# Optimization experiments

Hardware: AMD Instinct MI355X
Metric: run time of the kernel (lower is better)

The kernel has to match this reference:

```python
import jax, jax.numpy as jnp
import numpy as np
from jax import lax

C = 128
HEADS = 8
HID = 256  # int(C * 2.0)
B, H, W = 8, 128, 128
EPS_LN = 1e-5
EPS_NORM = 1e-12


def _dwconv(x, w, pad):
    # x: [B,C,H,W], w: [C,1,kh,kw] depthwise
    return lax.conv_general_dilated(
        x, w, window_strides=(1, 1), padding=[(pad, pad), (pad, pad)],
        dimension_numbers=("NCHW", "OIHW", "NCHW"), feature_group_count=x.shape[1])


def _conv1x1(x, w):
    # w: [O, I] pointwise conv
    return jnp.einsum("oi,bihw->bohw", w, x)


def _layernorm_c(x, gamma, beta):
    # torch: reshape to [B, HW, C], LayerNorm over C, reshape back == LN over channel axis
    mu = jnp.mean(x, axis=1, keepdims=True)
    var = jnp.mean(jnp.square(x - mu), axis=1, keepdims=True)
    xn = (x - mu) * lax.rsqrt(var + EPS_LN)
    return xn * gamma[None, :, None, None] + beta[None, :, None, None]


def _l2norm(x):
    n = jnp.sqrt(jnp.sum(jnp.square(x), axis=-1, keepdims=True))
    return x / jnp.maximum(n, EPS_NORM)


def _mdta(x, qkv_w, qkv_dw, temperature, attn_proj):
    b, c, h, w = x.shape
    qkv = _dwconv(_conv1x1(x, qkv_w), qkv_dw, pad=1)  # [B,3C,H,W]
    q, k, v = jnp.split(qkv, 3, axis=1)
    hd = c // HEADS
    q = q.reshape(b, HEADS, hd, h * w)
    k = k.reshape(b, HEADS, hd, h * w)
    v = v.reshape(b, HEADS, hd, h * w)
    q, k = _l2norm(q), _l2norm(k)
    attn = jax.nn.softmax(jnp.einsum("bhdn,bhen->bhde", q, k) * temperature, axis=-1)
    out = jnp.einsum("bhde,bhen->bhdn", attn, v).reshape(b, c, h, w)
    return _conv1x1(out, attn_proj)


def _gdfn2(x, pin_w, c1_w, c3_w, c5_w, pout_w):
    x = _conv1x1(x, pin_w)  # [B,HID,H,W]
    x1 = x * c1_w[None, :, 0, 0, 0, None, None]  # depthwise 1x1 == per-channel scale
    x3 = _dwconv(x, c3_w, pad=1)
    x5 = _dwconv(x, c5_w, pad=2)
    g = jax.nn.gelu(x1, approximate=False)
    gated = jnp.concatenate([g * x3, g * x5], axis=1)  # [B,2*HID,H,W]
    return _conv1x1(gated, pout_w)


def setup_inputs() -> dict:
    key = jax.random.key(0)
    ks = jax.random.split(key, 12)
    s = 0.05
    return {
        "x": jax.random.normal(ks[0], (B, C, H, W), jnp.float32),
        "ln1_w": jnp.ones((C,), jnp.float32),
        "ln1_b": jnp.zeros((C,), jnp.float32),
        "qkv_w": jax.random.normal(ks[1], (3 * C, C), jnp.float32) * s,
        "qkv_dw": jax.random.normal(ks[2], (3 * C, 1, 3, 3), jnp.float32) * s,
        "temperature": jnp.ones((1, HEADS, 1, 1), jnp.float32),
        "attn_proj": jax.random.normal(ks[3], (C, C), jnp.float32) * s,
        "ln2_w": jnp.ones((C,), jnp.float32),
        "ln2_b": jnp.zeros((C,), jnp.float32),
        "pin_w": jax.random.normal(ks[4], (HID, C), jnp.float32) * s,
        "c1_w": jax.random.normal(ks[5], (HID, 1, 1, 1), jnp.float32) * s,
        "c3_w": jax.random.normal(ks[6], (HID, 1, 3, 3), jnp.float32) * s,
        "c5_w": jax.random.normal(ks[7], (HID, 1, 5, 5), jnp.float32) * s,
        "pout_w": jax.random.normal(ks[8], (C, 2 * HID), jnp.float32) * s,
    }


def reference(x, ln1_w, ln1_b, qkv_w, qkv_dw, temperature, attn_proj,
              ln2_w, ln2_b, pin_w, c1_w, c3_w, c5_w, pout_w):
    x = x + _mdta(_layernorm_c(x, ln1_w, ln1_b), qkv_w, qkv_dw, temperature, attn_proj)
    x = x + _gdfn2(_layernorm_c(x, ln2_w, ln2_b), pin_w, c1_w, c3_w, c5_w, pout_w)
    return x
```

## Files before the change

kernel.cpp:

```cpp
#include <hip/hip_runtime.h>
#include <type_traits>

typedef unsigned short ushort;
typedef unsigned int uint;
typedef __bf16 bf16x8 __attribute__((ext_vector_type(8)));
typedef unsigned short ushort8v __attribute__((ext_vector_type(8)));
typedef float f32x4 __attribute__((ext_vector_type(4)));

__device__ __forceinline__ float b2f(ushort u) {
    unsigned int x = ((unsigned int)u) << 16;
    float f;
    __builtin_memcpy(&f, &x, 4);
    return f;
}
__device__ __forceinline__ ushort f2bf(float f) {
    unsigned int x;
    __builtin_memcpy(&x, &f, 4);
    unsigned int r = x + 0x7fffu + ((x >> 16) & 1u);
    return (ushort)(r >> 16);
}
__device__ __forceinline__ float u2f_lo(uint u) {
    uint x = u << 16;
    float f;
    __builtin_memcpy(&f, &x, 4);
    return f;
}
__device__ __forceinline__ float u2f_hi(uint u) {
    uint x = u & 0xffff0000u;
    float f;
    __builtin_memcpy(&f, &x, 4);
    return f;
}
__device__ __forceinline__ uint packbf(float a, float b) {
    return (uint)f2bf(a) | ((uint)f2bf(b) << 16);
}

#define NPIX 16384
#define PSTRIDE 136

__device__ __forceinline__ size_t tadr(int b, int CH, int tile, int ch, int off) {
    return (((size_t)b * 256 + tile) * CH + ch) * 64 + off;
}
__device__ __forceinline__ size_t padr(int b, int tile, int p, int c) {
    return (((size_t)b * 256 + tile) * 64 + p) * 128 + c;
}

__device__ __forceinline__ void stage_plane(ushort* pl, const ushort* __restrict__ src,
                                            int b, int c, int CH, int tid) {
    uint* plu = (uint*)pl;
    for (int i = tid; i < 784; i += 256) {
        int idx;
        if (i < 136) idx = i;
        else if (i < 272) idx = 8840 + (i - 136);
        else {
            int j = i - 272;
            int r = (j >> 2) + 2;
            int cs = j & 3;
            idx = r * 68 + (cs == 0 ? 0 : 64 + cs);
        }
        plu[idx] = 0u;
    }
    for (int i = tid; i < 2048; i += 256) {
        int row = i >> 4, xg = (i & 15) << 3;
        int px0 = row * 128 + xg;
        uint4 v = *(const uint4*)&src[tadr(b, CH, px0 >> 6, c, px0 & 63)];
        uint* dst = (uint*)&pl[(row + 2) * PSTRIDE + xg + 2];
        dst[0] = v.x; dst[1] = v.y; dst[2] = v.z; dst[3] = v.w;
    }
    __syncthreads();
}

__device__ __forceinline__ void unpack12(const ushort* rowp, float* cc) {
    const uint* rp = (const uint*)rowp;
    uint4 u = *(const uint4*)rp;
    uint2 v = *(const uint2*)(rp + 4);
    cc[0] = u2f_lo(u.x); cc[1] = u2f_hi(u.x);
    cc[2] = u2f_lo(u.y); cc[3] = u2f_hi(u.y);
    cc[4] = u2f_lo(u.z); cc[5] = u2f_hi(u.z);
    cc[6] = u2f_lo(u.w); cc[7] = u2f_hi(u.w);
    cc[8] = u2f_lo(v.x); cc[9] = u2f_hi(v.x);
    cc[10] = u2f_lo(v.y); cc[11] = u2f_hi(v.y);
}

__global__ __launch_bounds__(256) void wcvt(const float* __restrict__ s0, ushort* __restrict__ d0, int n0,
                                            const float* __restrict__ s1, ushort* __restrict__ d1, int n1,
                                            const float* __restrict__ s2, ushort* __restrict__ d2, int n2) {
    int i = blockIdx.x * 256 + threadIdx.x;
    if (i < n0) d0[i] = f2bf(s0[i]);
    else if (i < n0 + n1) d1[i - n0] = f2bf(s1[i - n0]);
    else if (i < n0 + n1 + n2) d2[i - n0 - n1] = f2bf(s2[i - n0 - n1]);
}

template <int O>
__global__ __launch_bounds__(256) void ln_gemm_mfma(const float* __restrict__ xin,
                                                    const ushort* __restrict__ Wb,
                                                    const float* __restrict__ gamma,
                                                    const float* __restrict__ beta,
                                                    ushort* __restrict__ out) {
    __shared__ ushort xs[64][136];
    __shared__ float red[2][4][64];
    __shared__ float mu[64], rs[64];
    __shared__ float gl[128], bl[128];

    const int blk = blockIdx.x;
    const int b = blk >> 8;
    const int tile = blk & 255;
    const int tid = threadIdx.x;

    const float* xb = xin + (size_t)b * 128 * NPIX + tile * 64;
    float vx[4][8];
#pragma unroll
    for (int k = 0; k < 4; k++) {
        int i = tid + k * 256;
        int p = i & 63, cg = i >> 6;
        const float* src = xb + (size_t)(cg * 8) * NPIX + p;
#pragma unroll
        for (int j = 0; j < 8; j++) vx[k][j] = src[(size_t)j * NPIX];
    }
    if (tid < 128) {
        gl[tid] = gamma[tid];
        bl[tid] = beta[tid];
    }
#pragma unroll
    for (int k = 0; k < 4; k++) {
        int i = tid + k * 256;
        int p = i & 63, cg = i >> 6;
        ushort8v u;
#pragma unroll
        for (int j = 0; j < 8; j++) u[j] = f2bf(vx[k][j]);
        *(ushort8v*)&xs[p][cg * 8] = u;
    }
    __syncthreads();

    {
        const int p = tid & 63, part = tid >> 6;
        float s = 0.f, ss = 0.f;
#pragma unroll
        for (int q = 0; q < 4; q++) {
            ushort8v u = *(const ushort8v*)&xs[p][part * 32 + q * 8];
#pragma unroll
            for (int j = 0; j < 8; j++) {
                float v = b2f(u[j]);
                s += v;
                ss += v * v;
            }
        }
        red[0][part][p] = s;
        red[1][part][p] = ss;
    }
    __syncthreads();
    if (tid < 64) {
        float s = red[0][0][tid] + red[0][1][tid] + red[0][2][tid] + red[0][3][tid];
        float ss = red[1][0][tid] + red[1][1][tid] + red[1][2][tid] + red[1][3][tid];
        float m = s * (1.f / 128.f);
        float var = ss * (1.f / 128.f) - m * m;
        mu[tid] = m;
        rs[tid] = rsqrtf(var + 1e-5f);
    }
    __syncthreads();
    {
        const int p = tid & 63, part = tid >> 6;
        const float mp = mu[p], rp = rs[p];
#pragma unroll
        for (int q = 0; q < 4; q++) {
            int c0 = part * 32 + q * 8;
            ushort8v u = *(const ushort8v*)&xs[p][c0];
            ushort8v o;
#pragma unroll
            for (int j = 0; j < 8; j++) {
                float v = b2f(u[j]);
                o[j] = f2bf((v - mp) * rp * gl[c0 + j] + bl[c0 + j]);
            }
            *(ushort8v*)&xs[p][c0] = o;
        }
    }
    __syncthreads();

    const int wv = tid >> 6, lane = tid & 63;
    const int lr = lane & 15, lg = lane >> 4;

    bf16x8 bfr[4][4];
#pragma unroll
    for (int t = 0; t < 4; t++)
#pragma unroll
        for (int kc = 0; kc < 4; kc++)
            bfr[t][kc] = __builtin_bit_cast(bf16x8, *(const ushort8v*)&xs[t * 16 + lr][kc * 32 + lg * 8]);

    constexpr int MT = O / 64;
    bf16x8 afp[2][4];
#pragma unroll
    for (int kc = 0; kc < 4; kc++)
        afp[0][kc] = __builtin_bit_cast(bf16x8,
            *(const ushort8v*)&Wb[(size_t)(wv * 16 + lr) * 128 + kc * 32 + lg * 8]);

    f32x4 accPair[2][4];
    const int px8 = tid & 7, cb = tid >> 3;
    ushort* outp = out + tadr(b, O, tile, 0, 0);

#pragma unroll
    for (int mt = 0; mt < MT; mt++) {
        if (mt + 1 < MT) {
            const int o0n = ((mt + 1) * 4 + wv) * 16;
#pragma unroll
            for (int kc = 0; kc < 4; kc++)
                afp[(mt + 1) & 1][kc] = __builtin_bit_cast(bf16x8,
                    *(const ushort8v*)&Wb[(size_t)(o0n + lr) * 128 + kc * 32 + lg * 8]);
        }
        f32x4* acc = accPair[mt & 1];
#pragma unroll
        for (int t = 0; t < 4; t++) acc[t] = (f32x4){0.f, 0.f, 0.f, 0.f};
#pragma unroll
        for (int kc = 0; kc < 4; kc++)
#pragma unroll
            for (int t = 0; t < 4; t++)
                acc[t] = __builtin_amdgcn_mfma_f32_16x16x32_bf16(afp[mt & 1][kc], bfr[t][kc], acc[t], 0, 0, 0);

        if (mt & 1) {
            __syncthreads();
#pragma unroll
            for (int h = 0; h < 2; h++) {
                const int lc = h * 64 + wv * 16 + lg * 4;
#pragma unroll
                for (int t = 0; t < 4; t++) {
                    int px = t * 16 + lr;
                    uint2 pk;
                    pk.x = packbf(accPair[h][t][0], accPair[h][t][1]);
                    pk.y = packbf(accPair[h][t][2], accPair[h][t][3]);
                    *(uint2*)&xs[px][lc] = pk;
                }
            }
            __syncthreads();
            const int pairbase = (mt >> 1) * 128;
#pragma unroll
            for (int cc = 0; cc < 4; cc++) {
                int c = cb + cc * 32;
                ushort8v u;
#pragma unroll
                for (int j = 0; j < 8; j++) u[j] = xs[px8 * 8 + j][c];
                *(ushort8v*)&outp[(size_t)(pairbase + c) * 64 + px8 * 8] = u;
            }
        }
    }
}

__global__ __launch_bounds__(256) void dwconv3_lds(const ushort* __restrict__ in,
                                                   const float* __restrict__ wdw,
                                                   ushort* __restrict__ out, int CH) {
    __shared__ ushort pl[132 * PSTRIDE];
    const int c = blockIdx.x;
    const int b = blockIdx.y;
    const int tid = threadIdx.x;

    float w[9];
#pragma unroll
    for (int j = 0; j < 9; j++) w[j] = wdw[c * 9 + j];

    stage_plane(pl, in, b, c, CH, tid);

    const int x = (tid & 15) * 8;
    const int ybase = tid >> 4;
#pragma unroll 1
    for (int k = 0; k < 8; k++) {
        const int y = k * 16 + ybase;
        float a[8];
#pragma unroll
        for (int p = 0; p < 8; p++) a[p] = 0.f;
#pragma unroll
        for (int ky = 0; ky < 3; ky++) {
            float cc[12];
            unpack12(&pl[(y + ky + 1) * PSTRIDE + x], cc);
#pragma unroll
            for (int kx = 0; kx < 3; kx++) {
                float wv = w[ky * 3 + kx];
#pragma unroll
                for (int p = 0; p < 8; p++) a[p] += cc[p + kx + 1] * wv;
            }
        }
        const int px0 = (y << 7) + x;
        uint4 o;
        o.x = packbf(a[0], a[1]);
        o.y = packbf(a[2], a[3]);
        o.z = packbf(a[4], a[5]);
        o.w = packbf(a[6], a[7]);
        *(uint4*)&out[tadr(b, CH, px0 >> 6, c, px0 & 63)] = o;
    }
}

__global__ __launch_bounds__(256) void dw_gated(const ushort* __restrict__ t,
                                                const float* __restrict__ w3_,
                                                const float* __restrict__ w5_,
                                                const float* __restrict__ c1w,
                                                ushort* __restrict__ gated) {
    __shared__ ushort pl[132 * PSTRIDE];
    const int c = blockIdx.x;
    const int b = blockIdx.y;
    const int tid = threadIdx.x;

    float w3[9], w5[25];
#pragma unroll
    for (int j = 0; j < 9; j++) w3[j] = w3_[c * 9 + j];
#pragma unroll
    for (int j = 0; j < 25; j++) w5[j] = w5_[c * 25 + j];
    const float c1v = c1w[c];

    stage_plane(pl, t, b, c, 256, tid);

    const int x = (tid & 15) * 8;
    const int ybase = tid >> 4;
#pragma unroll 1
    for (int k = 0; k < 8; k++) {
        const int y = k * 16 + ybase;
        float a5[8], a3[8], tc[8];
#pragma unroll
        for (int p = 0; p < 8; p++) { a5[p] = 0.f; a3[p] = 0.f; }
#pragma unroll
        for (int ky = 0; ky < 5; ky++) {
            float cc[12];
            unpack12(&pl[(y + ky) * PSTRIDE + x], cc);
#pragma unroll
            for (int kx = 0; kx < 5; kx++) {
                float wv = w5[ky * 5 + kx];
#pragma unroll
                for (int p = 0; p < 8; p++) a5[p] += cc[p + kx] * wv;
            }
            if (ky >= 1 && ky <= 3) {
#pragma unroll
                for (int kx = 0; kx < 3; kx++) {
                    float wv = w3[(ky - 1) * 3 + kx];
#pragma unroll
                    for (int p = 0; p < 8; p++) a3[p] += cc[p + kx + 1] * wv;
                }
            }
            if (ky == 2) {
#pragma unroll
                for (int p = 0; p < 8; p++) tc[p] = cc[p + 2];
            }
        }
        const int px0 = (y << 7) + x;
        uint4 o3, o5;
        float g[8];
#pragma unroll
        for (int p = 0; p < 8; p++) {
            float x1 = tc[p] * c1v;
            g[p] = x1 * __builtin_amdgcn_rcpf(1.f + __expf(-1.702f * x1));
        }
        o3.x = packbf(g[0] * a3[0], g[1] * a3[1]);
        o3.y = packbf(g[2] * a3[2], g[3] * a3[3]);
        o3.z = packbf(g[4] * a3[4], g[5] * a3[5]);
        o3.w = packbf(g[6] * a3[6], g[7] * a3[7]);
        o5.x = packbf(g[0] * a5[0], g[1] * a5[1]);
        o5.y = packbf(g[2] * a5[2], g[3] * a5[3]);
        o5.z = packbf(g[4] * a5[4], g[5] * a5[5]);
        o5.w = packbf(g[6] * a5[6], g[7] * a5[7]);
        *(uint4*)&gated[tadr(b, 512, px0 >> 6, c, px0 & 63)] = o3;
        *(uint4*)&gated[tadr(b, 512, px0 >> 6, 256 + c, px0 & 63)] = o5;
    }
}

__global__ __launch_bounds__(512) void attn_M(const ushort* __restrict__ qkv,
                                              const float* __restrict__ temp,
                                              const float* __restrict__ attn_proj,
                                              ushort* __restrict__ M) {
    __shared__ float Sp[8][16][16];
    __shared__ float QSS[8][16], KSS[8][16];
    __shared__ float A[16][17];

    const int bh = blockIdx.x, b = bh >> 3, h = bh & 7;
    const int tid = threadIdx.x;
    const int w = tid >> 6, lane = tid & 63;
    const int lr = lane & 15, lg = lane >> 4;

    const size_t qbase = (((size_t)b * 256 + w * 32) * 384 + h * 16 + lr) * 64 + lg * 8;
    const size_t kbase = qbase + (size_t)128 * 64;

    f32x4 acc = {0.f, 0.f, 0.f, 0.f};
    f32x4 accq = {0.f, 0.f, 0.f, 0.f};
    f32x4 acck = {0.f, 0.f, 0.f, 0.f};
#pragma unroll 2
    for (int it = 0; it < 64; it++) {
        size_t off = (size_t)(it >> 1) * (384 * 64) + (it & 1) * 32;
        bf16x8 qf = __builtin_bit_cast(bf16x8, *(const ushort8v*)(qkv + qbase + off));
        bf16x8 kf = __builtin_bit_cast(bf16x8, *(const ushort8v*)(qkv + kbase + off));
        acc = __builtin_amdgcn_mfma_f32_16x16x32_bf16(qf, kf, acc, 0, 0, 0);
        accq = __builtin_amdgcn_mfma_f32_16x16x32_bf16(qf, qf, accq, 0, 0, 0);
        acck = __builtin_amdgcn_mfma_f32_16x16x32_bf16(kf, kf, acck, 0, 0, 0);
    }
#pragma unroll
    for (int r = 0; r < 4; r++) Sp[w][lg * 4 + r][lr] = acc[r];
    if (lg == (lr >> 2)) {
        QSS[w][lr] = accq[lr & 3];
        KSS[w][lr] = acck[lr & 3];
    }
    __syncthreads();

    if (tid < 256) {
        const int d = tid >> 4, e = tid & 15;
        float S = 0.f, q2 = 0.f, k2 = 0.f;
#pragma unroll
        for (int s = 0; s < 8; s++) {
            S += Sp[s][d][e];
            q2 += QSS[s][d];
            k2 += KSS[s][e];
        }
        float nq = fmaxf(sqrtf(q2), 1e-12f);
        float nk = fmaxf(sqrtf(k2), 1e-12f);
        float logit = S / (nq * nk) * temp[h];
        float m = logit;
        for (int off = 8; off; off >>= 1) m = fmaxf(m, __shfl_xor(m, off, 64));
        float ex = expf(logit - m);
        float sum = ex;
        for (int off = 8; off; off >>= 1) sum += __shfl_xor(sum, off, 64);
        A[d][e] = ex / sum;
    }
    __syncthreads();

    for (int i = tid; i < 2048; i += 512) {
        int o = i >> 4, ee = i & 15;
        float acc2 = 0.f;
#pragma unroll
        for (int dd = 0; dd < 16; dd++) acc2 += attn_proj[o * 128 + h * 16 + dd] * A[dd][ee];
        M[((size_t)b * 128 + o) * 128 + h * 16 + ee] = f2bf(acc2);
    }
}

__global__ __launch_bounds__(256) void mv_ln_mfma(const ushort* __restrict__ qkv,
                                                  const ushort* __restrict__ Mb16,
                                                  const float* __restrict__ x,
                                                  const ushort* __restrict__ pin_b,
                                                  const float* __restrict__ gamma,
                                                  const float* __restrict__ beta,
                                                  ushort* __restrict__ x2,
                                                  ushort* __restrict__ t_out) {
    __shared__ ushort ts[64][136];
    __shared__ float red[2][4][64];
    __shared__ float mu[64], rs[64];
    __shared__ float gl[128], bl[128];

    const int blk = blockIdx.x;
    const int b = blk >> 8;
    const int tile = blk & 255;
    const int tid = threadIdx.x;
    const int wv = tid >> 6, lane = tid & 63;
    const int lr = lane & 15, lg = lane >> 4;

    const ushort* Mb = Mb16 + (size_t)b * 128 * 128;
    bf16x8 mfr[2][4];
#pragma unroll
    for (int mt = 0; mt < 2; mt++)
#pragma unroll
        for (int kc = 0; kc < 4; kc++)
            mfr[mt][kc] = __builtin_bit_cast(bf16x8,
                *(const ushort8v*)&Mb[(size_t)((wv * 2 + mt) * 16 + lr) * 128 + kc * 32 + lg * 8]);

    const ushort* vb = qkv + tadr(b, 384, tile, 256, 0);
    ushort8v vv[4];
#pragma unroll
    for (int k = 0; k < 4; k++) {
        int idx = tid + k * 256;
        int c = idx & 127, pg = idx >> 7;
        vv[k] = *(const ushort8v*)&vb[c * 64 + pg * 8];
    }
    if (tid < 128) {
        gl[tid] = gamma[tid];
        bl[tid] = beta[tid];
    }
#pragma unroll
    for (int k = 0; k < 4; k++) {
        int idx = tid + k * 256;
        int c = idx & 127, pg = idx >> 7;
#pragma unroll
        for (int j = 0; j < 8; j++) ts[pg * 8 + j][c] = vv[k][j];
    }
    __syncthreads();

    bf16x8 bfr[4][4];
#pragma unroll
    for (int t = 0; t < 4; t++)
#pragma unroll
        for (int kc = 0; kc < 4; kc++)
            bfr[t][kc] = __builtin_bit_cast(bf16x8, *(const ushort8v*)&ts[t * 16 + lr][kc * 32 + lg * 8]);
    __syncthreads();

#pragma unroll
    for (int mt = 0; mt < 2; mt++) {
        const int o0 = (wv * 2 + mt) * 16;
        f32x4 acc[4] = {{0.f, 0.f, 0.f, 0.f}, {0.f, 0.f, 0.f, 0.f}, {0.f, 0.f, 0.f, 0.f}, {0.f, 0.f, 0.f, 0.f}};
#pragma unroll
        for (int kc = 0; kc < 4; kc++)
#pragma unroll
            for (int t = 0; t < 4; t++)
                acc[t] = __builtin_amdgcn_mfma_f32_16x16x32_bf16(mfr[mt][kc], bfr[t][kc], acc[t], 0, 0, 0);
#pragma unroll
        for (int t = 0; t < 4; t++) {
            int px = t * 16 + lr;
            const float* xp = &x[((size_t)b * 128 + o0 + lg * 4) * NPIX + tile * 64 + px];
            uint2 pk;
            pk.x = packbf(xp[0] + acc[t][0], xp[NPIX] + acc[t][1]);
            pk.y = packbf(xp[2 * NPIX] + acc[t][2], xp[3 * NPIX] + acc[t][3]);
            *(uint2*)&ts[px][o0 + lg * 4] = pk;
        }
    }

    bf16x8 pfp[2][4];
#pragma unroll
    for (int kc = 0; kc < 4; kc++)
        pfp[0][kc] = __builtin_bit_cast(bf16x8,
            *(const ushort8v*)&pin_b[(size_t)(wv * 16 + lr) * 128 + kc * 32 + lg * 8]);
    __syncthreads();

#pragma unroll
    for (int k = 0; k < 4; k++) {
        int idx = tid + k * 256;
        int p = idx >> 4, seg = idx & 15;
        uint4 v = *(const uint4*)&ts[p][seg * 8];
        *(uint4*)&x2[padr(b, tile, p, seg * 8)] = v;
    }
    {
        const int p = tid & 63, part = tid >> 6;
        float s = 0.f, ss = 0.f;
#pragma unroll
        for (int q = 0; q < 4; q++) {
            ushort8v u = *(const ushort8v*)&ts[p][part * 32 + q * 8];
#pragma unroll
            for (int j = 0; j < 8; j++) {
                float v = b2f(u[j]);
                s += v;
                ss += v * v;
            }
        }
        red[0][part][p] = s;
        red[1][part][p] = ss;
    }
    __syncthreads();
    if (tid < 64) {
        float s = red[0][0][tid] + red[0][1][tid] + red[0][2][tid] + red[0][3][tid];
        float ss = red[1][0][tid] + red[1][1][tid] + red[1][2][tid] + red[1][3][tid];
        float m = s * (1.f / 128.f);
        float var = ss * (1.f / 128.f) - m * m;
        mu[tid] = m;
        rs[tid] = rsqrtf(var + 1e-5f);
    }
    __syncthreads();
    {
        const int p = tid & 63, part = tid >> 6;
        const float mp = mu[p], rp = rs[p];
#pragma unroll
        for (int q = 0; q < 4; q++) {
            int c0 = part * 32 + q * 8;
            ushort8v u = *(const ushort8v*)&ts[p][c0];
            ushort8v o;
#pragma unroll
            for (int j = 0; j < 8; j++) {
                float v = b2f(u[j]);
                o[j] = f2bf((v - mp) * rp * gl[c0 + j] + bl[c0 + j]);
            }
            *(ushort8v*)&ts[p][c0] = o;
        }
    }
    __syncthreads();

    bf16x8 bfr2[4][4];
#pragma unroll
    for (int t = 0; t < 4; t++)
#pragma unroll
        for (int kc = 0; kc < 4; kc++)
            bfr2[t][kc] = __builtin_bit_cast(bf16x8, *(const ushort8v*)&ts[t * 16 + lr][kc * 32 + lg * 8]);

    f32x4 accPair[2][4];
    const int px8 = tid & 7, cb = tid >> 3;
    ushort* toutp = t_out + tadr(b, 256, tile, 0, 0);

#pragma unroll
    for (int mt = 0; mt < 4; mt++) {
        if (mt + 1 < 4) {
            const int o0n = ((mt + 1) * 4 + wv) * 16;
#pragma unroll
            for (int kc = 0; kc < 4; kc++)
                pfp[(mt + 1) & 1][kc] = __builtin_bit_cast(bf16x8,
                    *(const ushort8v*)&pin_b[(size_t)(o0n + lr) * 128 + kc * 32 + lg * 8]);
        }
        f32x4* acc = accPair[mt & 1];
#pragma unroll
        for (int t = 0; t < 4; t++) acc[t] = (f32x4){0.f, 0.f, 0.f, 0.f};
#pragma unroll
        for (int kc = 0; kc < 4; kc++)
#pragma unroll
            for (int t = 0; t < 4; t++)
                acc[t] = __builtin_amdgcn_mfma_f32_16x16x32_bf16(pfp[mt & 1][kc], bfr2[t][kc], acc[t], 0, 0, 0);

        if (mt & 1) {
            __syncthreads();
#pragma unroll
            for (int h = 0; h < 2; h++) {
                const int lc = h * 64 + wv * 16 + lg * 4;
#pragma unroll
                for (int t = 0; t < 4; t++) {
                    int px = t * 16 + lr;
                    uint2 pk;
                    pk.x = packbf(accPair[h][t][0], accPair[h][t][1]);
                    pk.y = packbf(accPair[h][t][2], accPair[h][t][3]);
                    *(uint2*)&ts[px][lc] = pk;
                }
            }
            __syncthreads();
            const int pairbase = (mt >> 1) * 128;
#pragma unroll
            for (int cc = 0; cc < 4; cc++) {
                int c = cb + cc * 32;
                ushort8v u;
#pragma unroll
                for (int j = 0; j < 8; j++) u[j] = ts[px8 * 8 + j][c];
                *(ushort8v*)&toutp[(size_t)(pairbase + c) * 64 + px8 * 8] = u;
            }
        }
    }
}

__global__ __launch_bounds__(256) void gdfn_mfma(const ushort* __restrict__ gated,
                                                 const ushort* __restrict__ x2,
                                                 const ushort* __restrict__ pout_b,
                                                 float* __restrict__ out) {
    __shared__ ushort gs[2][64][72];
    float (*xf)[129] = (float(*)[129])gs;

    const int blk = blockIdx.x;
    const int b = blk >> 8;
    const int tile = blk & 255;
    const int tid = threadIdx.x;
    const int wv = tid >> 6, lane = tid & 63;
    const int lr = lane & 15, lg = lane >> 4;

    const ushort* gb = gated + tadr(b, 512, tile, 0, 0);
    const int p0 = tid & 63;
    const int kga = tid >> 6;

    f32x4 acc[2][4];
#pragma unroll
    for (int mt = 0; mt < 2; mt++)
#pragma unroll
        for (int tt = 0; tt < 4; tt++) acc[mt][tt] = (f32x4){0.f, 0.f, 0.f, 0.f};

    {
        ushort ca[8], cbv[8];
#pragma unroll
        for (int j = 0; j < 8; j++) ca[j] = gb[(kga * 8 + j) * 64 + p0];
#pragma unroll
        for (int j = 0; j < 8; j++) cbv[j] = gb[((kga + 4) * 8 + j) * 64 + p0];
        ushort8v ua, ub;
#pragma unroll
        for (int j = 0; j < 8; j++) { ua[j] = ca[j]; ub[j] = cbv[j]; }
        *(ushort8v*)&gs[0][p0][kga * 8] = ua;
        *(ushort8v*)&gs[0][p0][(kga + 4) * 8] = ub;
    }
    __syncthreads();

#pragma unroll
    for (int kb = 0; kb < 8; kb++) {
        const int cur = kb & 1;

        ushort na[8], nb[8];
        if (kb < 7) {
            const ushort* nbp = gb + (kb + 1) * 4096;
#pragma unroll
            for (int j = 0; j < 8; j++) na[j] = nbp[(kga * 8 + j) * 64 + p0];
#pragma unroll
            for (int j = 0; j < 8; j++) nb[j] = nbp[((kga + 4) * 8 + j) * 64 + p0];
        }

        bf16x8 bfrg[4][2];
#pragma unroll
        for (int tt = 0; tt < 4; tt++)
#pragma unroll
            for (int kc = 0; kc < 2; kc++)
                bfrg[tt][kc] = __builtin_bit_cast(bf16x8, *(const ushort8v*)&gs[cur][tt * 16 + lr][kc * 32 + lg * 8]);

#pragma unroll
        for (int mt = 0; mt < 2; mt++) {
            const int o0 = (wv * 2 + mt) * 16;
            bf16x8 afr[2];
#pragma unroll
            for (int kc = 0; kc < 2; kc++)
                afr[kc] = __builtin_bit_cast(bf16x8,
                    *(const ushort8v*)&pout_b[(size_t)(o0 + lr) * 512 + kb * 64 + kc * 32 + lg * 8]);
#pragma unroll
            for (int kc = 0; kc < 2; kc++)
#pragma unroll
                for (int tt = 0; tt < 4; tt++)
                    acc[mt][tt] = __builtin_amdgcn_mfma_f32_16x16x32_bf16(afr[kc], bfrg[tt][kc], acc[mt][tt], 0, 0, 0);
        }

        if (kb < 7) {
            ushort8v ua, ub;
#pragma unroll
            for (int j = 0; j < 8; j++) { ua[j] = na[j]; ub[j] = nb[j]; }
            *(ushort8v*)&gs[cur ^ 1][p0][kga * 8] = ua;
            *(ushort8v*)&gs[cur ^ 1][p0][(kga + 4) * 8] = ub;
        }
        __syncthreads();
    }

#pragma unroll
    for (int h = 0; h < 2; h++) {
#pragma unroll
        for (int mt = 0; mt < 2; mt++)
#pragma unroll
            for (int t2 = 0; t2 < 2; t2++) {
                const int tt = h * 2 + t2;
                int o0 = (wv * 2 + mt) * 16 + lg * 4;
                int px = tt * 16 + lr;
                uint2 xw = *(const uint2*)&x2[padr(b, tile, px, o0)];
                xf[px - h * 32][o0 + 0] = u2f_lo(xw.x) + acc[mt][tt][0];
                xf[px - h * 32][o0 + 1] = u2f_hi(xw.x) + acc[mt][tt][1];
                xf[px - h * 32][o0 + 2] = u2f_lo(xw.y) + acc[mt][tt][2];
                xf[px - h * 32][o0 + 3] = u2f_hi(xw.y) + acc[mt][tt][3];
            }
        __syncthreads();
        {
            const int qx = tid & 7;
            const int cbase = tid >> 3;
#pragma unroll
            for (int cc = 0; cc < 4; cc++) {
                int c = cbase + cc * 32;
                float4 v;
                v.x = xf[qx * 4 + 0][c];
                v.y = xf[qx * 4 + 1][c];
                v.z = xf[qx * 4 + 2][c];
                v.w = xf[qx * 4 + 3][c];
                *(float4*)&out[((size_t)b * 128 + c) * NPIX + tile * 64 + h * 32 + qx * 4] = v;
            }
        }
        __syncthreads();
    }
}

extern "C" void kernel_launch(void* const* d_in, const int* in_sizes, int n_in,
                              void* d_out, int out_size, void* d_ws, size_t ws_size,
                              hipStream_t stream) {
    const float* x = (const float*)d_in[0];
    const float* ln1_w = (const float*)d_in[1];
    const float* ln1_b = (const float*)d_in[2];
    const float* qkv_w = (const float*)d_in[3];
    const float* qkv_dw = (const float*)d_in[4];
    const float* temperature = (const float*)d_in[5];
    const float* attn_proj = (const float*)d_in[6];
    const float* ln2_w = (const float*)d_in[7];
    const float* ln2_b = (const float*)d_in[8];
    const float* pin_w = (const float*)d_in[9];
    const float* c1_w = (const float*)d_in[10];
    const float* c3_w = (const float*)d_in[11];
    const float* c5_w = (const float*)d_in[12];
    const float* pout_w = (const float*)d_in[13];
    float* out = (float*)d_out;

    char* ws = (char*)d_ws;
    ushort* qkv_pre = (ushort*)(ws + 0);
    ushort* qkv     = (ushort*)(ws + 100663296);
    ushort* x2      = (ushort*)(ws + 201326592);
    ushort* t       = (ushort*)(ws + 0);
    ushort* gated   = (ushort*)(ws + 67108864);
    ushort* Mb16    = (ushort*)(ws + 235151360);
    ushort* qkv_wb  = (ushort*)(ws + 235413504);
    ushort* pin_wb  = (ushort*)(ws + 235511808);
    ushort* pout_wb = (ushort*)(ws + 235577344);

    wcvt<<<576, 256, 0, stream>>>(qkv_w, qkv_wb, 49152, pin_w, pin_wb, 32768, pout_w, pout_wb, 65536);
    ln_gemm_mfma<384><<<2048, 256, 0, stream>>>(x, qkv_wb, ln1_w, ln1_b, qkv_pre);
    dwconv3_lds<<<dim3(384, 8), 256, 0, stream>>>(qkv_pre, qkv_dw, qkv, 384);
    attn_M<<<64, 512, 0, stream>>>(qkv, temperature, attn_proj, Mb16);
    mv_ln_mfma<<<2048, 256, 0, stream>>>(qkv, Mb16, x, pin_wb, ln2_w, ln2_b, x2, t);
    dw_gated<<<dim3(256, 8), 256, 0, stream>>>(t, c3_w, c5_w, c1_w, gated);
    gdfn_mfma<<<2048, 256, 0, stream>>>(gated, x2, pout_wb, out);
}
```

Baseline: 301.7 us.

## Re-layout gated buffer into 16-pixel chunks and use transposing LDS reads

The gated intermediate is now written with pixels grouped into 16-wide sub-tiles per channel, so the final projection kernel can stage each K-block with two 16-byte global loads per thread instead of sixteen scalar 2-byte loads. The MFMA B fragments are then built with ds_read_b64_tr_b16 transposing LDS reads rather than from a pixel-major padded tile. This targets the uncoalesced global gathers and the per-element LDS packing in the GDFN output projection. It relies on inline assembly, a full lgkmcnt wait and a scheduling barrier, which may limit overlap, and the layout change must match exactly between producer and consumer.

```diff
diff --git a/kernel.cpp b/kernel.cpp
--- a/kernel.cpp
+++ b/kernel.cpp
@@ -43,6 +43,9 @@
 }
 __device__ __forceinline__ size_t padr(int b, int tile, int p, int c) {
     return (((size_t)b * 256 + tile) * 64 + p) * 128 + c;
+}
+__device__ __forceinline__ size_t gadr(int b, int tile, int pxq, int ch, int pxl) {
+    return ((((size_t)b * 256 + tile) * 4 + pxq) * 512 + ch) * 16 + pxl;
 }
 
 __device__ __forceinline__ void stage_plane(ushort* pl, const ushort* __restrict__ src,
@@ -352,8 +355,9 @@
         o5.y = packbf(g[2] * a5[2], g[3] * a5[3]);
         o5.z = packbf(g[4] * a5[4], g[5] * a5[5]);
         o5.w = packbf(g[6] * a5[6], g[7] * a5[7]);
-        *(uint4*)&gated[tadr(b, 512, px0 >> 6, c, px0 & 63)] = o3;
-        *(uint4*)&gated[tadr(b, 512, px0 >> 6, 256 + c, px0 & 63)] = o5;
+        const int tl = px0 >> 6, pxq = (px0 >> 4) & 3, pxl = px0 & 15;
+        *(uint4*)&gated[gadr(b, tl, pxq, c, pxl)] = o3;
+        *(uint4*)&gated[gadr(b, tl, pxq, 256 + c, pxl)] = o5;
     }
 }
 
@@ -620,8 +624,10 @@
                                                  const ushort* __restrict__ x2,
                                                  const ushort* __restrict__ pout_b,
                                                  float* __restrict__ out) {
-    __shared__ ushort gs[2][64][72];
-    float (*xf)[129] = (float(*)[129])gs;
+    __shared__ union {
+        ushort gs[2][4096];
+        float xf[32][129];
+    } sm;
 
     const int blk = blockIdx.x;
     const int b = blk >> 8;
@@ -630,9 +636,11 @@
     const int wv = tid >> 6, lane = tid & 63;
     const int lr = lane & 15, lg = lane >> 4;
 
-    const ushort* gb = gated + tadr(b, 512, tile, 0, 0);
-    const int p0 = tid & 63;
-    const int kga = tid >> 6;
+    const ushort* gb = gated + gadr(b, tile, 0, 0, 0);
+    const int spxq = tid >> 6, scc = tid & 63;
+    const size_t sgoff = (size_t)spxq * 8192 + scc * 16;
+
+    const uint lbase = (uint)(uintptr_t)&sm.gs[0][0] + lg * 256 + lr * 2;
 
     f32x4 acc[2][4];
 #pragma unroll
@@ -641,16 +649,10 @@
         for (int tt = 0; tt < 4; tt++) acc[mt][tt] = (f32x4){0.f, 0.f, 0.f, 0.f};
 
     {
-        ushort ca[8], cbv[8];
-#pragma unroll
-        for (int j = 0; j < 8; j++) ca[j] = gb[(kga * 8 + j) * 64 + p0];
-#pragma unroll
-        for (int j = 0; j < 8; j++) cbv[j] = gb[((kga + 4) * 8 + j) * 64 + p0];
-        ushort8v ua, ub;
-#pragma unroll
-        for (int j = 0; j < 8; j++) { ua[j] = ca[j]; ub[j] = cbv[j]; }
-        *(ushort8v*)&gs[0][p0][kga * 8] = ua;
-        *(ushort8v*)&gs[0][p0][(kga + 4) * 8] = ub;
+        uint4 a0 = *(const uint4*)&gb[sgoff];
+        uint4 a1 = *(const uint4*)&gb[sgoff + 8];
+        *(uint4*)&sm.gs[0][tid * 16] = a0;
+        *(uint4*)&sm.gs[0][tid * 16 + 8] = a1;
     }
     __syncthreads();
 
@@ -658,21 +660,31 @@
     for (int kb = 0; kb < 8; kb++) {
         const int cur = kb & 1;
 
-        ushort na[8], nb[8];
+        uint4 nA, nB;
         if (kb < 7) {
-            const ushort* nbp = gb + (kb + 1) * 4096;
-#pragma unroll
-            for (int j = 0; j < 8; j++) na[j] = nbp[(kga * 8 + j) * 64 + p0];
-#pragma unroll
-            for (int j = 0; j < 8; j++) nb[j] = nbp[((kga + 4) * 8 + j) * 64 + p0];
+            nA = *(const uint4*)&gb[sgoff + (kb + 1) * 1024];
+            nB = *(const uint4*)&gb[sgoff + (kb + 1) * 1024 + 8];
         }
 
         bf16x8 bfrg[4][2];
-#pragma unroll
-        for (int tt = 0; tt < 4; tt++)
-#pragma unroll
-            for (int kc = 0; kc < 2; kc++)
-                bfrg[tt][kc] = __builtin_bit_cast(bf16x8, *(const ushort8v*)&gs[cur][tt * 16 + lr][kc * 32 + lg * 8]);
+        {
+            const uint la = lbase + cur * 8192;
+#pragma unroll
+            for (int tt = 0; tt < 4; tt++)
+#pragma unroll
+                for (int kc = 0; kc < 2; kc++) {
+                    uint2 r0, r1;
+                    asm volatile("ds_read_b64_tr_b16 %0, %2 offset:%3\n\t"
+                                 "ds_read_b64_tr_b16 %1, %2 offset:%4"
+                                 : "=&v"(r0), "=&v"(r1)
+                                 : "v"(la), "i"(tt * 2048 + kc * 1024), "i"(tt * 2048 + kc * 1024 + 128));
+                    uint4 q;
+                    q.x = r0.x; q.y = r0.y; q.z = r1.x; q.w = r1.y;
+                    bfrg[tt][kc] = __builtin_bit_cast(bf16x8, q);
+                }
+        }
+        asm volatile("s_waitcnt lgkmcnt(0)" ::: "memory");
+        __builtin_amdgcn_sched_barrier(0);
 
 #pragma unroll
         for (int mt = 0; mt < 2; mt++) {
@@ -690,11 +702,8 @@
         }
 
         if (kb < 7) {
-            ushort8v ua, ub;
-#pragma unroll
-            for (int j = 0; j < 8; j++) { ua[j] = na[j]; ub[j] = nb[j]; }
-            *(ushort8v*)&gs[cur ^ 1][p0][kga * 8] = ua;
-            *(ushort8v*)&gs[cur ^ 1][p0][(kga + 4) * 8] = ub;
+            *(uint4*)&sm.gs[cur ^ 1][tid * 16] = nA;
+            *(uint4*)&sm.gs[cur ^ 1][tid * 16 + 8] = nB;
         }
         __syncthreads();
     }
@@ -709,10 +718,10 @@
                 int o0 = (wv * 2 + mt) * 16 + lg * 4;
                 int px = tt * 16 + lr;
                 uint2 xw = *(const uint2*)&x2[padr(b, tile, px, o0)];
-                xf[px - h * 32][o0 + 0] = u2f_lo(xw.x) + acc[mt][tt][0];
-                xf[px - h * 32][o0 + 1] = u2f_hi(xw.x) + acc[mt][tt][1];
-                xf[px - h * 32][o0 + 2] = u2f_lo(xw.y) + acc[mt][tt][2];
-                xf[px - h * 32][o0 + 3] = u2f_hi(xw.y) + acc[mt][tt][3];
+                sm.xf[px - h * 32][o0 + 0] = u2f_lo(xw.x) + acc[mt][tt][0];
+                sm.xf[px - h * 32][o0 + 1] = u2f_hi(xw.x) + acc[mt][tt][1];
+                sm.xf[px - h * 32][o0 + 2] = u2f_lo(xw.y) + acc[mt][tt][2];
+                sm.xf[px - h * 32][o0 + 3] = u2f_hi(xw.y) + acc[mt][tt][3];
             }
         __syncthreads();
         {
@@ -722,10 +731,10 @@
             for (int cc = 0; cc < 4; cc++) {
                 int c = cbase + cc * 32;
                 float4 v;
-                v.x = xf[qx * 4 + 0][c];
-                v.y = xf[qx * 4 + 1][c];
-                v.z = xf[qx * 4 + 2][c];
-                v.w = xf[qx * 4 + 3][c];
+                v.x = sm.xf[qx * 4 + 0][c];
+                v.y = sm.xf[qx * 4 + 1][c];
+                v.z = sm.xf[qx * 4 + 2][c];
+                v.w = sm.xf[qx * 4 + 3][c];
                 *(float4*)&out[((size_t)b * 128 + c) * NPIX + tile * 64 + h * 32 + qx * 4] = v;
             }
         }
```

Result: slower. 315.0 us (+4.4%).
